# Optimization experiments

Hardware: AMD Instinct MI355X
Metric: run time of the kernel (lower is better)

## Reference

```python
import jax, jax.numpy as jnp
import numpy as np

N, IN_DIM, KEY_DIM, K, VAL_DIM = 100000, 512, 100, 8, 64


def setup_inputs() -> dict:
    key = jax.random.key(0)
    ks = jax.random.split(key, 7)
    s = 0.02
    return {
        "x": jax.random.normal(ks[0], (N, IN_DIM), dtype=jnp.float32),
        "Wk": jax.random.normal(ks[1], (KEY_DIM, IN_DIM), dtype=jnp.float32) * s,
        "bk": jax.random.normal(ks[2], (KEY_DIM,), dtype=jnp.float32) * s,
        "Wq": jax.random.normal(ks[3], (K, KEY_DIM), dtype=jnp.float32) * s,
        "bq": jax.random.normal(ks[4], (K,), dtype=jnp.float32) * s,
        "Wv": jax.random.normal(ks[5], (VAL_DIM, IN_DIM), dtype=jnp.float32) * s,
        "bv": jax.random.normal(ks[6], (VAL_DIM,), dtype=jnp.float32) * s,
    }


def reference(x, Wk, bk, Wq, bq, Wv, bv):
    # torch.nn.Linear: y = x @ W.T + b
    key = x @ Wk.T + bk                  # [N, key_dim]
    val = x @ Wv.T + bv                  # [N, val_dim]
    que = key @ Wq.T + bq                # [N, k]
    # att_norm == 'softmax': per-sample softmax over the k groups
    w = jax.nn.softmax(que, axis=-1)     # [N, k]
    # per-sample outer product w_i^T @ val_i -> [N, k, val_dim]
    x_group = w[:, :, None] * val[:, None, :]
    return x_group
```

## Files before the change

### kernel.cpp

```cpp
#include <hip/hip_runtime.h>

#define NROWS 100000
#define IN_DIM 512

typedef __attribute__((ext_vector_type(8))) short short8;
typedef __attribute__((ext_vector_type(4))) float f32x4;

__device__ inline unsigned short f2bf(float f) {
    union { float f; unsigned u; } v; v.f = f;
    unsigned u = v.u;
    return (unsigned short)((u + 0x7FFFu + ((u >> 16) & 1u)) >> 16);
}

__global__ void qg_prepack(const float* __restrict__ Wk, const float* __restrict__ bk,
                           const float* __restrict__ Wq, const float* __restrict__ bq,
                           const float* __restrict__ Wv,
                           unsigned short* __restrict__ Bp, float* __restrict__ qb) {
    int id = blockIdx.x * 256 + threadIdx.x;
    if (id < 8) {
        float s = bq[id];
        #pragma unroll 4
        for (int j = 0; j < 100; ++j) s += Wq[id * 100 + j] * bk[j];
        qb[id] = s;
    }
    if (id >= 5120) return;
    int lane = id & 63;
    int ks = (id >> 6) & 15;
    int t = id >> 10;
    int c = t * 16 + (lane & 15);
    int kk = ks * 32 + (lane >> 4) * 8;
    short8 pk;
    #pragma unroll
    for (int e = 0; e < 8; ++e) {
        int k2 = kk + e;
        float w;
        if (c < 64) {
            w = Wv[c * IN_DIM + k2];
        } else if (c < 72) {
            float s = 0.f;
            #pragma unroll 4
            for (int j = 0; j < 100; ++j) s += Wq[(c - 64) * 100 + j] * Wk[j * IN_DIM + k2];
            w = s;
        } else {
            w = 0.f;
        }
        pk[e] = (short)f2bf(w);
    }
    ((short8*)Bp)[id] = pk;
}

__global__ __launch_bounds__(128, 4) void qg_main(const float* __restrict__ x,
                                                  const float* __restrict__ bv,
                                                  const unsigned short* __restrict__ Bp,
                                                  const float* __restrict__ qb,
                                                  float* __restrict__ out) {
    __shared__ float vlds[2][16][68];
    __shared__ float wlds[2][16][8];
    const int tid = threadIdx.x;
    const int w = tid >> 6;
    const int lane = tid & 63;
    const int g = lane >> 4;
    const int cl = lane & 15;
    const int rowbase = blockIdx.x * 32 + w * 16;

    const float* ap = x + (size_t)(rowbase + cl) * IN_DIM + g * 8;
    const short8* bp8 = (const short8*)Bp + lane;

    f32x4 acc[5];
    #pragma unroll
    for (int t = 0; t < 5; ++t) acc[t] = (f32x4){0.f, 0.f, 0.f, 0.f};

    float4 A[3][2];
    short8 B[2][5];

    #pragma unroll
    for (int p = 0; p < 3; ++p) {
        A[p][0] = *(const float4*)(ap + p * 32);
        A[p][1] = *(const float4*)(ap + p * 32 + 4);
    }
    #pragma unroll
    for (int p = 0; p < 2; ++p)
        #pragma unroll
        for (int t = 0; t < 5; ++t)
            B[p][t] = bp8[(t * 16 + p) * 64];

    #pragma unroll
    for (int s = 0; s < 16; ++s) {
        const int ai = s % 3, bi = s % 2;
        float4 f0 = A[ai][0];
        float4 f1 = A[ai][1];
        short8 af;
        af[0] = (short)f2bf(f0.x); af[1] = (short)f2bf(f0.y);
        af[2] = (short)f2bf(f0.z); af[3] = (short)f2bf(f0.w);
        af[4] = (short)f2bf(f1.x); af[5] = (short)f2bf(f1.y);
        af[6] = (short)f2bf(f1.z); af[7] = (short)f2bf(f1.w);
        if (s + 3 < 16) {
            A[ai][0] = *(const float4*)(ap + (s + 3) * 32);
            A[ai][1] = *(const float4*)(ap + (s + 3) * 32 + 4);
        }
        #pragma unroll
        for (int t = 0; t < 5; ++t)
            acc[t] = __builtin_amdgcn_mfma_f32_16x16x32_bf16(af, B[bi][t], acc[t], 0, 0, 0);
        if (s + 2 < 16) {
            #pragma unroll
            for (int t = 0; t < 5; ++t)
                B[bi][t] = bp8[(t * 16 + s + 2) * 64];
        }
    }

    #pragma unroll
    for (int t = 0; t < 4; ++t) {
        float b = bv[t * 16 + cl];
        #pragma unroll
        for (int r = 0; r < 4; ++r)
            vlds[w][g * 4 + r][t * 16 + cl] = acc[t][r] + b;
    }
    if (cl < 8) {
        float b = qb[cl];
        #pragma unroll
        for (int r = 0; r < 4; ++r)
            wlds[w][g * 4 + r][cl] = acc[4][r] + b;
    }
    asm volatile("s_waitcnt lgkmcnt(0)" ::: "memory");

    if (lane < 16) {
        float q[8];
        float m = -1e30f;
        #pragma unroll
        for (int k = 0; k < 8; ++k) { q[k] = wlds[w][lane][k]; m = fmaxf(m, q[k]); }
        float ssum = 0.f;
        #pragma unroll
        for (int k = 0; k < 8; ++k) { q[k] = __expf(q[k] - m); ssum += q[k]; }
        float inv = 1.f / ssum;
        #pragma unroll
        for (int k = 0; k < 8; ++k) wlds[w][lane][k] = q[k] * inv;
    }
    asm volatile("s_waitcnt lgkmcnt(0)" ::: "memory");

    f32x4* outp = (f32x4*)out + (size_t)rowbase * 128;
    #pragma unroll
    for (int it = 0; it < 32; ++it) {
        int idx = it * 64 + lane;
        int row = idx >> 7;
        int j = idx & 127;
        float wgt = wlds[w][row][j >> 4];
        float4 vv = *(const float4*)&vlds[w][row][(j & 15) * 4];
        f32x4 o;
        o[0] = wgt * vv.x; o[1] = wgt * vv.y; o[2] = wgt * vv.z; o[3] = wgt * vv.w;
        __builtin_nontemporal_store(o, &outp[(size_t)row * 128 + j]);
    }
}

extern "C" void kernel_launch(void* const* d_in, const int* in_sizes, int n_in,
                              void* d_out, int out_size, void* d_ws, size_t ws_size,
                              hipStream_t stream) {
    const float* x  = (const float*)d_in[0];
    const float* Wk = (const float*)d_in[1];
    const float* bk = (const float*)d_in[2];
    const float* Wq = (const float*)d_in[3];
    const float* bq = (const float*)d_in[4];
    const float* Wv = (const float*)d_in[5];
    const float* bv = (const float*)d_in[6];
    float* out = (float*)d_out;

    unsigned short* Bp = (unsigned short*)d_ws;
    float* qb = (float*)((char*)d_ws + 81920);

    qg_prepack<<<20, 256, 0, stream>>>(Wk, bk, Wq, bq, Wv, Bp, qb);
    qg_main<<<3125, 128, 0, stream>>>(x, bv, Bp, qb, out);
}
```

Baseline: 107.1 us.

## Hand-schedule global loads with inline asm and deeper prefetch, use 256-thread blocks

Replaces compiler-generated loads of x and packed weights with inline-asm global_load_dwordx4 using scalar base plus vector offset. Loads run a 3-stage-deep prefetch ring with explicit vmcnt waits and sched barriers around the MFMA steps. Bias loads are hoisted ahead of the loop. Blocks grow to 4 waves covering 64 rows, so 1563 blocks are launched, with clamped input rows and guarded stores for the tail. This aims to keep more memory requests in flight while streaming x, at the cost of higher register pressure and fragile manual wait counts.

Result: faster. 102.0 us (-4.7%).

```diff
diff --git a/kernel.cpp b/kernel.cpp
--- a/kernel.cpp
+++ b/kernel.cpp
@@ -49,77 +49,99 @@
     ((short8*)Bp)[id] = pk;
 }
 
-__global__ __launch_bounds__(128, 4) void qg_main(const float* __restrict__ x,
+__global__ __launch_bounds__(256, 2) void qg_main(const float* __restrict__ x,
                                                   const float* __restrict__ bv,
                                                   const unsigned short* __restrict__ Bp,
                                                   const float* __restrict__ qb,
                                                   float* __restrict__ out) {
-    __shared__ float vlds[2][16][68];
-    __shared__ float wlds[2][16][8];
+    __shared__ float vlds[4][16][68];
+    __shared__ float wlds[4][16][8];
     const int tid = threadIdx.x;
     const int w = tid >> 6;
     const int lane = tid & 63;
     const int g = lane >> 4;
     const int cl = lane & 15;
-    const int rowbase = blockIdx.x * 32 + w * 16;
+    const int rowbase = blockIdx.x * 64 + w * 16;
+    const int arow = min(rowbase + cl, NROWS - 1);
 
-    const float* ap = x + (size_t)(rowbase + cl) * IN_DIM + g * 8;
-    const short8* bp8 = (const short8*)Bp + lane;
+    const unsigned voffA = (unsigned)(arow * 512 + g * 8) * 4u;
+    const unsigned voffB = (unsigned)lane * 16u;
 
+    float bvr[4];
+    #pragma unroll
+    for (int t = 0; t < 4; ++t) bvr[t] = bv[t * 16 + cl];
+    float qbr = qb[cl & 7];
+    asm volatile("s_waitcnt vmcnt(0)" ::: "memory");
+
+    f32x4 A0[4], A1[4];
+    short8 Bv[4][5];
     f32x4 acc[5];
     #pragma unroll
     for (int t = 0; t < 5; ++t) acc[t] = (f32x4){0.f, 0.f, 0.f, 0.f};
 
-    float4 A[3][2];
-    short8 B[2][5];
+#define GLD(dst, off, base, IMM)                                               \
+    asm volatile("global_load_dwordx4 %0, %1, %2 offset:" IMM                  \
+                 : "=&v"(dst) : "v"(off), "s"(base) : "memory")
 
-    #pragma unroll
-    for (int p = 0; p < 3; ++p) {
-        A[p][0] = *(const float4*)(ap + p * 32);
-        A[p][1] = *(const float4*)(ap + p * 32 + 4);
-    }
-    #pragma unroll
-    for (int p = 0; p < 2; ++p)
-        #pragma unroll
-        for (int t = 0; t < 5; ++t)
-            B[p][t] = bp8[(t * 16 + p) * 64];
+#define ISSUE(S) do {                                                          \
+        unsigned va_ = voffA + (S) * 128u;                                     \
+        GLD(A0[(S) & 3], va_, x, "0");                                         \
+        GLD(A1[(S) & 3], va_, x, "16");                                        \
+        GLD(Bv[(S) & 3][0], voffB + (0 * 16 + (S)) * 1024u, Bp, "0");          \
+        GLD(Bv[(S) & 3][1], voffB + (1 * 16 + (S)) * 1024u, Bp, "0");          \
+        GLD(Bv[(S) & 3][2], voffB + (2 * 16 + (S)) * 1024u, Bp, "0");          \
+        GLD(Bv[(S) & 3][3], voffB + (3 * 16 + (S)) * 1024u, Bp, "0");          \
+        GLD(Bv[(S) & 3][4], voffB + (4 * 16 + (S)) * 1024u, Bp, "0");          \
+    } while (0)
 
-    #pragma unroll
-    for (int s = 0; s < 16; ++s) {
-        const int ai = s % 3, bi = s % 2;
-        float4 f0 = A[ai][0];
-        float4 f1 = A[ai][1];
-        short8 af;
-        af[0] = (short)f2bf(f0.x); af[1] = (short)f2bf(f0.y);
-        af[2] = (short)f2bf(f0.z); af[3] = (short)f2bf(f0.w);
-        af[4] = (short)f2bf(f1.x); af[5] = (short)f2bf(f1.y);
-        af[6] = (short)f2bf(f1.z); af[7] = (short)f2bf(f1.w);
-        if (s + 3 < 16) {
-            A[ai][0] = *(const float4*)(ap + (s + 3) * 32);
-            A[ai][1] = *(const float4*)(ap + (s + 3) * 32 + 4);
-        }
-        #pragma unroll
-        for (int t = 0; t < 5; ++t)
-            acc[t] = __builtin_amdgcn_mfma_f32_16x16x32_bf16(af, B[bi][t], acc[t], 0, 0, 0);
-        if (s + 2 < 16) {
-            #pragma unroll
-            for (int t = 0; t < 5; ++t)
-                B[bi][t] = bp8[(t * 16 + s + 2) * 64];
-        }
-    }
+#define CONSUME(S, NW) do {                                                    \
+        asm volatile("s_waitcnt vmcnt(" NW ")" ::: "memory");                  \
+        __builtin_amdgcn_sched_barrier(0);                                     \
+        f32x4 f0_ = A0[(S) & 3];                                               \
+        f32x4 f1_ = A1[(S) & 3];                                               \
+        short8 af_;                                                            \
+        af_[0] = (short)f2bf(f0_[0]); af_[1] = (short)f2bf(f0_[1]);            \
+        af_[2] = (short)f2bf(f0_[2]); af_[3] = (short)f2bf(f0_[3]);            \
+        af_[4] = (short)f2bf(f1_[0]); af_[5] = (short)f2bf(f1_[1]);            \
+        af_[6] = (short)f2bf(f1_[2]); af_[7] = (short)f2bf(f1_[3]);            \
+        acc[0] = __builtin_amdgcn_mfma_f32_16x16x32_bf16(af_, Bv[(S)&3][0], acc[0], 0, 0, 0); \
+        acc[1] = __builtin_amdgcn_mfma_f32_16x16x32_bf16(af_, Bv[(S)&3][1], acc[1], 0, 0, 0); \
+        acc[2] = __builtin_amdgcn_mfma_f32_16x16x32_bf16(af_, Bv[(S)&3][2], acc[2], 0, 0, 0); \
+        acc[3] = __builtin_amdgcn_mfma_f32_16x16x32_bf16(af_, Bv[(S)&3][3], acc[3], 0, 0, 0); \
+        acc[4] = __builtin_amdgcn_mfma_f32_16x16x32_bf16(af_, Bv[(S)&3][4], acc[4], 0, 0, 0); \
+    } while (0)
+
+    ISSUE(0); ISSUE(1); ISSUE(2);
+    CONSUME(0, "14");  ISSUE(3);
+    CONSUME(1, "14");  ISSUE(4);
+    CONSUME(2, "14");  ISSUE(5);
+    CONSUME(3, "14");  ISSUE(6);
+    CONSUME(4, "14");  ISSUE(7);
+    CONSUME(5, "14");  ISSUE(8);
+    CONSUME(6, "14");  ISSUE(9);
+    CONSUME(7, "14");  ISSUE(10);
+    CONSUME(8, "14");  ISSUE(11);
+    CONSUME(9, "14");  ISSUE(12);
+    CONSUME(10, "14"); ISSUE(13);
+    CONSUME(11, "14"); ISSUE(14);
+    CONSUME(12, "14"); ISSUE(15);
+    CONSUME(13, "14");
+    CONSUME(14, "7");
+    CONSUME(15, "0");
+#undef GLD
+#undef ISSUE
+#undef CONSUME
 
     #pragma unroll
     for (int t = 0; t < 4; ++t) {
-        float b = bv[t * 16 + cl];
         #pragma unroll
         for (int r = 0; r < 4; ++r)
-            vlds[w][g * 4 + r][t * 16 + cl] = acc[t][r] + b;
+            vlds[w][g * 4 + r][t * 16 + cl] = acc[t][r] + bvr[t];
     }
     if (cl < 8) {
-        float b = qb[cl];
         #pragma unroll
         for (int r = 0; r < 4; ++r)
-            wlds[w][g * 4 + r][cl] = acc[4][r] + b;
+            wlds[w][g * 4 + r][cl] = acc[4][r] + qbr;
     }
     asm volatile("s_waitcnt lgkmcnt(0)" ::: "memory");
 
@@ -143,11 +165,13 @@
         int idx = it * 64 + lane;
         int row = idx >> 7;
         int j = idx & 127;
-        float wgt = wlds[w][row][j >> 4];
-        float4 vv = *(const float4*)&vlds[w][row][(j & 15) * 4];
-        f32x4 o;
-        o[0] = wgt * vv.x; o[1] = wgt * vv.y; o[2] = wgt * vv.z; o[3] = wgt * vv.w;
-        __builtin_nontemporal_store(o, &outp[(size_t)row * 128 + j]);
+        if (rowbase + row < NROWS) {
+            float wgt = wlds[w][row][j >> 4];
+            float4 vv = *(const float4*)&vlds[w][row][(j & 15) * 4];
+            f32x4 o;
+            o[0] = wgt * vv.x; o[1] = wgt * vv.y; o[2] = wgt * vv.z; o[3] = wgt * vv.w;
+            __builtin_nontemporal_store(o, &outp[(size_t)row * 128 + j]);
+        }
     }
 }
 
@@ -167,5 +191,5 @@
     float* qb = (float*)((char*)d_ws + 81920);
 
     qg_prepack<<<20, 256, 0, stream>>>(Wk, bk, Wq, bq, Wv, Bp, qb);
-    qg_main<<<3125, 128, 0, stream>>>(x, bv, Bp, qb, out);
+    qg_main<<<1563, 256, 0, stream>>>(x, bv, Bp, qb, out);
 }
```

## Stage x tiles and packed weights into LDS via direct global-to-LDS loads

Applied to the files above, without the earlier changes.

Replaces the register-pipelined global loads of x and the packed weight matrix with direct global_load_lds transfers into a large shared buffer. Each block loads the full 80 KB packed B matrix plus a 16x512 x tile per wave, using an XOR swizzle to avoid bank conflicts, then runs the MFMA loop from LDS. The aim is fewer VGPRs spent on in-flight loads and wider, more coalesced memory transactions. The cost is about 144 KB of LDS per block, which limits occupancy to one block per CU and removes overlap between loading and compute inside a block.

New measurement: 120.9 us. +12.9%, slower.

```diff
diff --git a/kernel.cpp b/kernel.cpp
--- a/kernel.cpp
+++ b/kernel.cpp
@@ -5,6 +5,9 @@
 
 typedef __attribute__((ext_vector_type(8))) short short8;
 typedef __attribute__((ext_vector_type(4))) float f32x4;
+typedef unsigned int u32;
+typedef const __attribute__((address_space(1))) u32* gptr_t;
+typedef __attribute__((address_space(3))) u32* lptr_t;
 
 __device__ inline unsigned short f2bf(float f) {
     union { float f; unsigned u; } v; v.f = f;
@@ -49,77 +52,87 @@
     ((short8*)Bp)[id] = pk;
 }
 
-__global__ __launch_bounds__(128, 4) void qg_main(const float* __restrict__ x,
+__global__ __launch_bounds__(128, 1) void qg_main(const float* __restrict__ x,
                                                   const float* __restrict__ bv,
                                                   const unsigned short* __restrict__ Bp,
                                                   const float* __restrict__ qb,
                                                   float* __restrict__ out) {
-    __shared__ float vlds[2][16][68];
-    __shared__ float wlds[2][16][8];
+    __shared__ float smem[36864];
     const int tid = threadIdx.x;
     const int w = tid >> 6;
     const int lane = tid & 63;
     const int g = lane >> 4;
     const int cl = lane & 15;
-    const int rowbase = blockIdx.x * 32 + w * 16;
+    const int rowbase = (blockIdx.x * 2 + w) * 16;
 
-    const float* ap = x + (size_t)(rowbase + cl) * IN_DIM + g * 8;
-    const short8* bp8 = (const short8*)Bp + lane;
+    float* Bls = smem;
+    float* tile = smem + 20480 + w * 8192;
+
+    float bvr[4];
+    #pragma unroll
+    for (int t = 0; t < 4; ++t) bvr[t] = bv[t * 16 + cl];
+    float qbr = qb[cl & 7];
+    asm volatile("s_waitcnt vmcnt(0)" ::: "memory");
+
+    #pragma unroll
+    for (int j = 0; j < 40; ++j) {
+        const int slot = w * 2560 + j * 64;
+        const char* src = (const char*)Bp + ((size_t)(slot + lane)) * 16;
+        __builtin_amdgcn_global_load_lds((gptr_t)(const void*)src,
+                                         (lptr_t)(void*)(Bls + (size_t)slot * 4), 16, 0, 0);
+    }
+    __builtin_amdgcn_sched_barrier(0);
+
+    #pragma unroll
+    for (int i = 0; i < 32; ++i) {
+        const int row = i >> 1;
+        const int c = (((i & 1) * 64) + lane) ^ (row & 7);
+        const float* src = x + (size_t)(rowbase + row) * IN_DIM + c * 4;
+        __builtin_amdgcn_global_load_lds((gptr_t)(const void*)src,
+                                         (lptr_t)(void*)(tile + i * 256), 16, 0, 0);
+    }
+    __builtin_amdgcn_sched_barrier(0);
+
+    asm volatile("s_waitcnt vmcnt(32)" ::: "memory");
+    __builtin_amdgcn_s_barrier();
+    asm volatile("s_waitcnt vmcnt(0)" ::: "memory");
+    __builtin_amdgcn_sched_barrier(0);
 
     f32x4 acc[5];
     #pragma unroll
     for (int t = 0; t < 5; ++t) acc[t] = (f32x4){0.f, 0.f, 0.f, 0.f};
-
-    float4 A[3][2];
-    short8 B[2][5];
-
-    #pragma unroll
-    for (int p = 0; p < 3; ++p) {
-        A[p][0] = *(const float4*)(ap + p * 32);
-        A[p][1] = *(const float4*)(ap + p * 32 + 4);
-    }
-    #pragma unroll
-    for (int p = 0; p < 2; ++p)
-        #pragma unroll
-        for (int t = 0; t < 5; ++t)
-            B[p][t] = bp8[(t * 16 + p) * 64];
+    const float4* t4 = (const float4*)tile;
+    const short8* b8 = (const short8*)Bls;
 
     #pragma unroll
     for (int s = 0; s < 16; ++s) {
-        const int ai = s % 3, bi = s % 2;
-        float4 f0 = A[ai][0];
-        float4 f1 = A[ai][1];
+        const int c0 = (s * 8 + g * 2)     ^ (cl & 7);
+        const int c1 = (s * 8 + g * 2 + 1) ^ (cl & 7);
+        float4 f0 = t4[cl * 128 + c0];
+        float4 f1 = t4[cl * 128 + c1];
         short8 af;
         af[0] = (short)f2bf(f0.x); af[1] = (short)f2bf(f0.y);
         af[2] = (short)f2bf(f0.z); af[3] = (short)f2bf(f0.w);
         af[4] = (short)f2bf(f1.x); af[5] = (short)f2bf(f1.y);
         af[6] = (short)f2bf(f1.z); af[7] = (short)f2bf(f1.w);
-        if (s + 3 < 16) {
-            A[ai][0] = *(const float4*)(ap + (s + 3) * 32);
-            A[ai][1] = *(const float4*)(ap + (s + 3) * 32 + 4);
-        }
         #pragma unroll
         for (int t = 0; t < 5; ++t)
-            acc[t] = __builtin_amdgcn_mfma_f32_16x16x32_bf16(af, B[bi][t], acc[t], 0, 0, 0);
-        if (s + 2 < 16) {
-            #pragma unroll
-            for (int t = 0; t < 5; ++t)
-                B[bi][t] = bp8[(t * 16 + s + 2) * 64];
-        }
+            acc[t] = __builtin_amdgcn_mfma_f32_16x16x32_bf16(af, b8[(t * 16 + s) * 64 + lane], acc[t], 0, 0, 0);
     }
 
+    asm volatile("s_waitcnt lgkmcnt(0)" ::: "memory");
+    float (*vld)[68] = (float(*)[68])tile;
+    float (*wld)[8]  = (float(*)[8])(tile + 16 * 68);
     #pragma unroll
     for (int t = 0; t < 4; ++t) {
-        float b = bv[t * 16 + cl];
         #pragma unroll
         for (int r = 0; r < 4; ++r)
-            vlds[w][g * 4 + r][t * 16 + cl] = acc[t][r] + b;
+            vld[g * 4 + r][t * 16 + cl] = acc[t][r] + bvr[t];
     }
     if (cl < 8) {
-        float b = qb[cl];
         #pragma unroll
         for (int r = 0; r < 4; ++r)
-            wlds[w][g * 4 + r][cl] = acc[4][r] + b;
+            wld[g * 4 + r][cl] = acc[4][r] + qbr;
     }
     asm volatile("s_waitcnt lgkmcnt(0)" ::: "memory");
 
@@ -127,13 +140,13 @@
         float q[8];
         float m = -1e30f;
         #pragma unroll
-        for (int k = 0; k < 8; ++k) { q[k] = wlds[w][lane][k]; m = fmaxf(m, q[k]); }
+        for (int k = 0; k < 8; ++k) { q[k] = wld[lane][k]; m = fmaxf(m, q[k]); }
         float ssum = 0.f;
         #pragma unroll
         for (int k = 0; k < 8; ++k) { q[k] = __expf(q[k] - m); ssum += q[k]; }
         float inv = 1.f / ssum;
         #pragma unroll
-        for (int k = 0; k < 8; ++k) wlds[w][lane][k] = q[k] * inv;
+        for (int k = 0; k < 8; ++k) wld[lane][k] = q[k] * inv;
     }
     asm volatile("s_waitcnt lgkmcnt(0)" ::: "memory");
 
@@ -143,8 +156,8 @@
         int idx = it * 64 + lane;
         int row = idx >> 7;
         int j = idx & 127;
-        float wgt = wlds[w][row][j >> 4];
-        float4 vv = *(const float4*)&vlds[w][row][(j & 15) * 4];
+        float wgt = wld[row][j >> 4];
+        float4 vv = *(const float4*)&vld[row][(j & 15) * 4];
         f32x4 o;
         o[0] = wgt * vv.x; o[1] = wgt * vv.y; o[2] = wgt * vv.z; o[3] = wgt * vv.w;
         __builtin_nontemporal_store(o, &outp[(size_t)row * 128 + j]);
```

## Hand-schedule main GEMM loop in inline asm with hardware bf16 conversion

Applied to the files above, without the earlier changes.

Replaces the compiler-scheduled K-loop with hand-written inline assembly that pins A/B buffers and accumulators to fixed VGPRs. It runs a triple-buffered global-load pipeline with explicit vmcnt waits and uses v_cvt_pk_bf16_f32 in place of the software rounding routine. Bias loads are hoisted before the loop and launch bounds drop from 4 to 2 blocks per CU, which may lower occupancy. Hard-coded VGPR numbers and fixed wait counts are fragile: correctness depends on the compiler not using those registers elsewhere.

Result: faster. 101.8 us (-4.9%).

```diff
diff --git a/kernel.cpp b/kernel.cpp
--- a/kernel.cpp
+++ b/kernel.cpp
@@ -49,7 +49,59 @@
     ((short8*)Bp)[id] = pk;
 }
 
-__global__ __launch_bounds__(128, 4) void qg_main(const float* __restrict__ x,
+#define CA0 "v48","v49","v50","v51","v52","v53","v54","v55"
+#define CA1 "v56","v57","v58","v59","v60","v61","v62","v63"
+#define CA2 "v64","v65","v66","v67","v68","v69","v70","v71"
+#define CB0 "v72","v73","v74","v75","v76","v77","v78","v79","v80","v81","v82","v83","v84","v85","v86","v87","v88","v89","v90","v91"
+#define CB1 "v92","v93","v94","v95","v96","v97","v98","v99","v100","v101","v102","v103","v104","v105","v106","v107","v108","v109","v110","v111"
+#define CB2 "v112","v113","v114","v115","v116","v117","v118","v119","v120","v121","v122","v123","v124","v125","v126","v127","v128","v129","v130","v131"
+#define COFF "v132","v133","v134","v135","v136","v137"
+#define CACC "v140","v141","v142","v143","v144","v145","v146","v147","v148","v149","v150","v151","v152","v153","v154","v155","v156","v157","v158","v159"
+
+#define ISSUE(AR0, AR1, B0, B1, B2, B3, B4, CLA, CLB)                          \
+    asm volatile(                                                              \
+        "global_load_dwordx4 " AR0 ", v132, %0 offset:0\n\t"                   \
+        "global_load_dwordx4 " AR1 ", v132, %0 offset:16\n\t"                  \
+        "v_add_u32 v132, 0x80, v132\n\t"                                       \
+        "global_load_dwordx4 " B0 ", v133, %1 offset:0\n\t"                    \
+        "v_add_u32 v133, 0x400, v133\n\t"                                      \
+        "global_load_dwordx4 " B1 ", v134, %1 offset:0\n\t"                    \
+        "v_add_u32 v134, 0x400, v134\n\t"                                      \
+        "global_load_dwordx4 " B2 ", v135, %1 offset:0\n\t"                    \
+        "v_add_u32 v135, 0x400, v135\n\t"                                      \
+        "global_load_dwordx4 " B3 ", v136, %1 offset:0\n\t"                    \
+        "v_add_u32 v136, 0x400, v136\n\t"                                      \
+        "global_load_dwordx4 " B4 ", v137, %1 offset:0\n\t"                    \
+        "v_add_u32 v137, 0x400, v137"                                          \
+        :: "s"(x), "s"(Bp) : "memory", CLA, CLB, COFF)
+
+#define ISSUE0 ISSUE("v[48:51]", "v[52:55]", "v[72:75]", "v[76:79]", "v[80:83]", "v[84:87]", "v[88:91]", CA0, CB0)
+#define ISSUE1 ISSUE("v[56:59]", "v[60:63]", "v[92:95]", "v[96:99]", "v[100:103]", "v[104:107]", "v[108:111]", CA1, CB1)
+#define ISSUE2 ISSUE("v[64:67]", "v[68:71]", "v[112:115]", "v[116:119]", "v[120:123]", "v[124:127]", "v[128:131]", CA2, CB2)
+
+#define CONS(NW, A0s, A1s, A2s, A3s, AF, B0, B1, B2, B3, B4, CLA)              \
+    asm volatile("s_waitcnt vmcnt(" NW ")" ::: "memory");                      \
+    asm volatile(                                                              \
+        "v_cvt_pk_bf16_f32 " A0s "\n\t"                                        \
+        "v_cvt_pk_bf16_f32 " A1s "\n\t"                                        \
+        "v_cvt_pk_bf16_f32 " A2s "\n\t"                                        \
+        "v_cvt_pk_bf16_f32 " A3s "\n\t"                                        \
+        "s_nop 1\n\t"                                                          \
+        "v_mfma_f32_16x16x32_bf16 v[140:143], " AF ", " B0 ", v[140:143]\n\t"  \
+        "v_mfma_f32_16x16x32_bf16 v[144:147], " AF ", " B1 ", v[144:147]\n\t"  \
+        "v_mfma_f32_16x16x32_bf16 v[148:151], " AF ", " B2 ", v[148:151]\n\t"  \
+        "v_mfma_f32_16x16x32_bf16 v[152:155], " AF ", " B3 ", v[152:155]\n\t"  \
+        "v_mfma_f32_16x16x32_bf16 v[156:159], " AF ", " B4 ", v[156:159]"      \
+        ::: "memory", CLA, CACC)
+
+#define CONS0(NW) CONS(NW, "v48, v48, v49", "v49, v50, v51", "v50, v52, v53", "v51, v54, v55", \
+                       "v[48:51]", "v[72:75]", "v[76:79]", "v[80:83]", "v[84:87]", "v[88:91]", CA0)
+#define CONS1(NW) CONS(NW, "v56, v56, v57", "v57, v58, v59", "v58, v60, v61", "v59, v62, v63", \
+                       "v[56:59]", "v[92:95]", "v[96:99]", "v[100:103]", "v[104:107]", "v[108:111]", CA1)
+#define CONS2(NW) CONS(NW, "v64, v64, v65", "v65, v66, v67", "v66, v68, v69", "v67, v70, v71", \
+                       "v[64:67]", "v[112:115]", "v[116:119]", "v[120:123]", "v[124:127]", "v[128:131]", CA2)
+
+__global__ __launch_bounds__(128, 2) void qg_main(const float* __restrict__ x,
                                                   const float* __restrict__ bv,
                                                   const unsigned short* __restrict__ Bp,
                                                   const float* __restrict__ qb,
@@ -61,65 +113,86 @@
     const int lane = tid & 63;
     const int g = lane >> 4;
     const int cl = lane & 15;
-    const int rowbase = blockIdx.x * 32 + w * 16;
-
-    const float* ap = x + (size_t)(rowbase + cl) * IN_DIM + g * 8;
-    const short8* bp8 = (const short8*)Bp + lane;
-
-    f32x4 acc[5];
-    #pragma unroll
-    for (int t = 0; t < 5; ++t) acc[t] = (f32x4){0.f, 0.f, 0.f, 0.f};
-
-    float4 A[3][2];
-    short8 B[2][5];
-
-    #pragma unroll
-    for (int p = 0; p < 3; ++p) {
-        A[p][0] = *(const float4*)(ap + p * 32);
-        A[p][1] = *(const float4*)(ap + p * 32 + 4);
-    }
-    #pragma unroll
-    for (int p = 0; p < 2; ++p)
-        #pragma unroll
-        for (int t = 0; t < 5; ++t)
-            B[p][t] = bp8[(t * 16 + p) * 64];
-
-    #pragma unroll
-    for (int s = 0; s < 16; ++s) {
-        const int ai = s % 3, bi = s % 2;
-        float4 f0 = A[ai][0];
-        float4 f1 = A[ai][1];
-        short8 af;
-        af[0] = (short)f2bf(f0.x); af[1] = (short)f2bf(f0.y);
-        af[2] = (short)f2bf(f0.z); af[3] = (short)f2bf(f0.w);
-        af[4] = (short)f2bf(f1.x); af[5] = (short)f2bf(f1.y);
-        af[6] = (short)f2bf(f1.z); af[7] = (short)f2bf(f1.w);
-        if (s + 3 < 16) {
-            A[ai][0] = *(const float4*)(ap + (s + 3) * 32);
-            A[ai][1] = *(const float4*)(ap + (s + 3) * 32 + 4);
-        }
-        #pragma unroll
-        for (int t = 0; t < 5; ++t)
-            acc[t] = __builtin_amdgcn_mfma_f32_16x16x32_bf16(af, B[bi][t], acc[t], 0, 0, 0);
-        if (s + 2 < 16) {
-            #pragma unroll
-            for (int t = 0; t < 5; ++t)
-                B[bi][t] = bp8[(t * 16 + s + 2) * 64];
-        }
-    }
+    const int rowbase = (blockIdx.x * 2 + w) * 16;
+
+    const unsigned voffA = (unsigned)((rowbase + cl) * 512 + g * 8) * 4u;
+    const unsigned voffB = (unsigned)lane * 16u;
+
+    float bvr[4];
+    #pragma unroll
+    for (int t = 0; t < 4; ++t) bvr[t] = bv[t * 16 + cl];
+    float qbr = qb[cl & 7];
+    asm volatile("s_waitcnt vmcnt(0)" ::: "memory");
+
+    asm volatile(
+        "v_mov_b32 v132, %0\n\t"
+        "v_mov_b32 v133, %1\n\t"
+        "v_mov_b32 v134, %2\n\t"
+        "v_mov_b32 v135, %3\n\t"
+        "v_mov_b32 v136, %4\n\t"
+        "v_mov_b32 v137, %5"
+        :: "v"(voffA), "v"(voffB), "v"(voffB + 16384u), "v"(voffB + 32768u),
+           "v"(voffB + 49152u), "v"(voffB + 65536u)
+        : COFF);
+    asm volatile(
+        "v_mov_b32 v140, 0\n\tv_mov_b32 v141, 0\n\tv_mov_b32 v142, 0\n\tv_mov_b32 v143, 0\n\t"
+        "v_mov_b32 v144, 0\n\tv_mov_b32 v145, 0\n\tv_mov_b32 v146, 0\n\tv_mov_b32 v147, 0\n\t"
+        "v_mov_b32 v148, 0\n\tv_mov_b32 v149, 0\n\tv_mov_b32 v150, 0\n\tv_mov_b32 v151, 0\n\t"
+        "v_mov_b32 v152, 0\n\tv_mov_b32 v153, 0\n\tv_mov_b32 v154, 0\n\tv_mov_b32 v155, 0\n\t"
+        "v_mov_b32 v156, 0\n\tv_mov_b32 v157, 0\n\tv_mov_b32 v158, 0\n\tv_mov_b32 v159, 0"
+        ::: CACC);
+
+    ISSUE0; ISSUE1; ISSUE2;
+    CONS0("14"); ISSUE0;
+    CONS1("14"); ISSUE1;
+    CONS2("14"); ISSUE2;
+    CONS0("14"); ISSUE0;
+    CONS1("14"); ISSUE1;
+    CONS2("14"); ISSUE2;
+    CONS0("14"); ISSUE0;
+    CONS1("14"); ISSUE1;
+    CONS2("14"); ISSUE2;
+    CONS0("14"); ISSUE0;
+    CONS1("14"); ISSUE1;
+    CONS2("14"); ISSUE2;
+    CONS0("14"); ISSUE0;
+    CONS1("14");
+    CONS2("7");
+    CONS0("0");
+
+    asm volatile("s_nop 7\n\ts_nop 7\n\ts_nop 7");
+    float ac[5][4];
+    asm volatile("v_mov_b32 %0, v140" : "=v"(ac[0][0]));
+    asm volatile("v_mov_b32 %0, v141" : "=v"(ac[0][1]));
+    asm volatile("v_mov_b32 %0, v142" : "=v"(ac[0][2]));
+    asm volatile("v_mov_b32 %0, v143" : "=v"(ac[0][3]));
+    asm volatile("v_mov_b32 %0, v144" : "=v"(ac[1][0]));
+    asm volatile("v_mov_b32 %0, v145" : "=v"(ac[1][1]));
+    asm volatile("v_mov_b32 %0, v146" : "=v"(ac[1][2]));
+    asm volatile("v_mov_b32 %0, v147" : "=v"(ac[1][3]));
+    asm volatile("v_mov_b32 %0, v148" : "=v"(ac[2][0]));
+    asm volatile("v_mov_b32 %0, v149" : "=v"(ac[2][1]));
+    asm volatile("v_mov_b32 %0, v150" : "=v"(ac[2][2]));
+    asm volatile("v_mov_b32 %0, v151" : "=v"(ac[2][3]));
+    asm volatile("v_mov_b32 %0, v152" : "=v"(ac[3][0]));
+    asm volatile("v_mov_b32 %0, v153" : "=v"(ac[3][1]));
+    asm volatile("v_mov_b32 %0, v154" : "=v"(ac[3][2]));
+    asm volatile("v_mov_b32 %0, v155" : "=v"(ac[3][3]));
+    asm volatile("v_mov_b32 %0, v156" : "=v"(ac[4][0]));
+    asm volatile("v_mov_b32 %0, v157" : "=v"(ac[4][1]));
+    asm volatile("v_mov_b32 %0, v158" : "=v"(ac[4][2]));
+    asm volatile("v_mov_b32 %0, v159" : "=v"(ac[4][3]));
 
     #pragma unroll
     for (int t = 0; t < 4; ++t) {
-        float b = bv[t * 16 + cl];
         #pragma unroll
         for (int r = 0; r < 4; ++r)
-            vlds[w][g * 4 + r][t * 16 + cl] = acc[t][r] + b;
+            vlds[w][g * 4 + r][t * 16 + cl] = ac[t][r] + bvr[t];
     }
     if (cl < 8) {
-        float b = qb[cl];
         #pragma unroll
         for (int r = 0; r < 4; ++r)
-            wlds[w][g * 4 + r][cl] = acc[4][r] + b;
+            wlds[w][g * 4 + r][cl] = ac[4][r] + qbr;
     }
     asm volatile("s_waitcnt lgkmcnt(0)" ::: "memory");
 
```
